# Performance work log

Hardware: AMD Instinct MI355X
Metric: run time of the kernel (lower is better)

Reference implementation:

```python
import jax, jax.numpy as jnp
import numpy as np

B, P, K_NN, HEADS = 4, 2048, 30, 3
N = B * P


def knn_nbr(feat):
    """Per-cloud exact KNN (no self), returns [N, K_NN+1] global neighbor idx, self appended last.
    Matches torch_geometric knn_graph (loop=False) followed by GATConv add_self_loops=True."""
    f = feat.reshape(B, P, -1)
    sq = jnp.sum(f * f, axis=-1)  # [B,P]
    d = sq[:, :, None] + sq[:, None, :] - 2.0 * jnp.einsum('bpc,bqc->bpq', f, f)
    d = d + jnp.eye(P, dtype=f.dtype)[None] * 1e9  # exclude self
    idx = jax.lax.top_k(-d, K_NN)[1]  # [B,P,K_NN] nearest neighbors
    idx = (idx + (jnp.arange(B) * P)[:, None, None]).reshape(N, K_NN)
    return jnp.concatenate([idx, jnp.arange(N)[:, None]], axis=1)  # self-loop last


def gat(xf, nbr, W, a_src, a_dst, bias):
    """PyG GATConv (v1, concat=True, negative_slope=0.2). nbr: [N,K] incoming sources per node."""
    H, F = a_src.shape
    xh = (xf @ W).reshape(N, H, F)
    s = jnp.sum(xh * a_src, axis=-1)  # [N,H] source scores
    t = jnp.sum(xh * a_dst, axis=-1)  # [N,H] target scores
    e = jax.nn.leaky_relu(s[nbr] + t[:, None, :], 0.2)  # [N,K,H]
    alpha = jax.nn.softmax(e, axis=1)  # edge-softmax over incoming edges
    out = jnp.einsum('nkh,nkhf->nhf', alpha, xh[nbr])
    return out.reshape(N, H * F) + bias


def setup_inputs() -> dict:
    key = jax.random.key(0)
    ks = jax.random.split(key, 48)
    w = lambda k, shape: (jax.random.normal(k, shape, jnp.float32) * 0.1)
    H = HEADS
    inp = {
        'x': jax.random.normal(ks[0], (N, 3), jnp.float32),
        'pos': jax.random.normal(ks[1], (N, 3), jnp.float32),
        'batch': (jnp.arange(N) // P).astype(jnp.int32),
        'w1': w(ks[2], (6, 64 * H)), 'as1': w(ks[3], (H, 64)), 'ad1': w(ks[4], (H, 64)), 'b1': w(ks[5], (64 * H,)),
        'ml1w': w(ks[6], (64 * H, 64)), 'ml1b': w(ks[7], (64,)),
        'w2': w(ks[8], (70, 64 * H)), 'as2': w(ks[9], (H, 64)), 'ad2': w(ks[10], (H, 64)), 'b2': w(ks[11], (64 * H,)),
        'ml2w': w(ks[12], (64 * H, 64)), 'ml2b': w(ks[13], (64,)),
        'w3': w(ks[14], (134, 64 * H)), 'as3': w(ks[15], (H, 64)), 'ad3': w(ks[16], (H, 64)), 'b3': w(ks[17], (64 * H,)),
        'ml3w': w(ks[18], (64 * H, 64)), 'ml3b': w(ks[19], (64,)),
        'w4': w(ks[20], (198, 128 * H)), 'as4': w(ks[21], (H, 128)), 'ad4': w(ks[22], (H, 128)), 'b4': w(ks[23], (128 * H,)),
        'ml4w': w(ks[24], (128 * H, 128)), 'ml4b': w(ks[25], (128,)),
        # fe_mlp: 326 -> 1024 -> 1024 (plain last)
        'few1': w(ks[26], (326, 1024)), 'feb1': w(ks[27], (1024,)),
        'few2': w(ks[28], (1024, 1024)), 'feb2': w(ks[29], (1024,)),
        # head mlp: 1350 -> 256 -> 256 -> 128 -> 50
        'mw1': w(ks[30], (1350, 256)), 'mb1': w(ks[31], (256,)),
        'mw2': w(ks[32], (256, 256)), 'mb2': w(ks[33], (256,)),
        'mw3': w(ks[34], (256, 128)), 'mb3': w(ks[35], (128,)),
        'mw4': w(ks[36], (128, 50)), 'mb4': w(ks[37], (50,)),
    }
    return inp


def reference(x, pos, batch,
              w1, as1, ad1, b1, ml1w, ml1b,
              w2, as2, ad2, b2, ml2w, ml2b,
              w3, as3, ad3, b3, ml3w, ml3b,
              w4, as4, ad4, b4, ml4w, ml4b,
              few1, feb1, few2, feb2,
              mw1, mb1, mw2, mb2, mw3, mb3, mw4, mb4):
    x0 = jnp.concatenate([x, pos], axis=-1)  # [N,6]
    nbr = knn_nbr(x0)
    x1 = gat(x0, nbr, w1, as1, ad1, b1) @ ml1w + ml1b  # [N,64]
    nbr = knn_nbr(x1)
    x2 = gat(jnp.concatenate([x0, x1], 1), nbr, w2, as2, ad2, b2) @ ml2w + ml2b
    nbr = knn_nbr(x2)
    x3 = gat(jnp.concatenate([x0, x1, x2], 1), nbr, w3, as3, ad3, b3) @ ml3w + ml3b
    nbr = knn_nbr(x2)  # faithful to source: 4th graph also built from x2
    x4 = gat(jnp.concatenate([x0, x1, x2, x3], 1), nbr, w4, as4, ad4, b4) @ ml4w + ml4b
    link4 = jnp.concatenate([x0, x1, x2, x3, x4], axis=-1)  # [N,326]
    h = jax.nn.relu(link4 @ few1 + feb1) @ few2 + feb2  # [N,1024]
    g = jnp.max(h, axis=0, keepdims=True)  # global feature (dropout=eval identity)
    lg = jnp.concatenate([link4, jnp.broadcast_to(g, (N, h.shape[1]))], axis=1)
    h = jax.nn.relu(lg @ mw1 + mb1)
    h = jax.nn.relu(h @ mw2 + mb2)
    h = jax.nn.relu(h @ mw3 + mb3)
    out = h @ mw4 + mb4
    return jax.nn.log_softmax(out, axis=1)
```

## Files before the change

kernel.cpp:

```cpp
#include <hip/hip_runtime.h>
#include <hip/hip_bf16.h>
#include <hip/amd_detail/amd_hip_vector_types.h>

#define NPTS 8192
#define PP 2048
#define KNN 30
#define KTOT 31
#define HEADS 3
#define LDH 352
#define NSEG 9
#define LDZ 200
#define LDZB3 200
#define LDZB4 392

typedef __attribute__((ext_vector_type(8))) short short8;
typedef __attribute__((ext_vector_type(4))) float floatx4;
typedef __attribute__((ext_vector_type(4))) unsigned int uint4_t;
typedef unsigned short ushort_t;
typedef unsigned int uint_t;

__device__ inline ushort_t f2bs(float v) {
    __hip_bfloat16 b = __float2bfloat16(v);
    return *reinterpret_cast<ushort_t*>(&b);
}
__device__ inline float bs2f(ushort_t u) {
    __hip_bfloat16 b = *reinterpret_cast<__hip_bfloat16*>(&u);
    return __bfloat162float(b);
}
__device__ inline void split2(float v, ushort_t& h, ushort_t& l) {
    h = f2bs(v);
    l = f2bs(v - bs2f(h));
}
__device__ inline uint_t fenc(float f) {
    uint_t b = __float_as_uint(f);
    return (b & 0x80000000u) ? ~b : (b | 0x80000000u);
}
__device__ inline float fdec(uint_t e) {
    return __uint_as_float((e & 0x80000000u) ? (e & 0x7FFFFFFFu) : ~e);
}

__global__ void k_build_x0(const float* __restrict__ x, const float* __restrict__ pos,
                           ushort_t* __restrict__ lh, ushort_t* __restrict__ ll) {
    int i = blockIdx.x * blockDim.x + threadIdx.x;
    if (i >= NPTS * 6) return;
    int n = i / 6, c = i % 6;
    float v = (c < 3) ? x[n * 3 + c] : pos[n * 3 + (c - 3)];
    ushort_t h, l; split2(v, h, l);
    lh[(size_t)n * LDH + c] = h;
    ll[(size_t)n * LDH + c] = l;
}

template<int F_>
__device__ inline void combine_body(const float* __restrict__ w, const float* __restrict__ mlw,
                                    const float* __restrict__ as_, const float* __restrict__ ad,
                                    const float* __restrict__ b, const float* __restrict__ mlb,
                                    float* __restrict__ wc, float* __restrict__ bc,
                                    int K_, int lb) {
    constexpr int NC = 3 * F_ + 6;
    constexpr int JG = 128 / F_;
    constexpr int RG = 8 / JG;
    int h = lb % 3, kb = lb / 3;
    int k0 = kb * 8, KS = min(8, K_ - k0);
    int tid = threadIdx.x;
    int j = tid % F_, rg = tid / F_;
    __shared__ float ws[8][F_];
    __shared__ float ms[32][F_];
    __shared__ float bav[3][F_];
    for (int idx = tid; idx < 8 * F_; idx += 128) {
        int r = idx / F_, f = idx % F_;
        ws[r][f] = (r < KS) ? w[(size_t)(k0 + r) * (3 * F_) + h * F_ + f] : 0.f;
    }
    for (int f = tid; f < F_; f += 128) {
        bav[0][f] = b[h * F_ + f];
        bav[1][f] = as_[h * F_ + f];
        bav[2][f] = ad[h * F_ + f];
    }
    __syncthreads();
    const float* mh = mlw + (size_t)h * F_ * F_;
    float acc[RG] = {};
    float bacc = 0.f;
    for (int f0 = 0; f0 < F_; f0 += 32) {
        for (int idx = tid; idx < 32 * F_; idx += 128) {
            int u = idx / F_, jj = idx % F_;
            ms[u][jj] = mh[(size_t)(f0 + u) * F_ + jj];
        }
        __syncthreads();
#pragma unroll
        for (int u = 0; u < 32; u++) {
            float m = ms[u][j];
#pragma unroll
            for (int r = 0; r < RG; r++)
                acc[r] += ws[rg * RG + r][f0 + u] * m;
            if (rg == 0) bacc += bav[0][f0 + u] * m;
        }
        __syncthreads();
    }
#pragma unroll
    for (int r = 0; r < RG; r++) {
        int k = k0 + rg * RG + r;
        if (k < K_) wc[(size_t)k * NC + h * F_ + j] = acc[r];
    }
    if (kb == 0 && rg == 0)
        atomicAdd(&bc[j], bacc + (h == 0 ? mlb[j] : 0.f));
    if (tid < 16) {
        int r = tid >> 1, sc = tid & 1;
        if (r < KS) {
            float s = 0.f;
#pragma unroll
            for (int f = 0; f < F_; f++) s += ws[r][f] * bav[1 + sc][f];
            wc[(size_t)(k0 + r) * NC + 3 * F_ + sc * 3 + h] = s;
        }
    }
}

struct CAll {
    const float *w[4], *mlw[4], *as_[4], *ad[4], *b[4], *mlb[4];
    float *wc[4], *bc[4];
    int K[4], t0[4], t64;
};
__global__ __launch_bounds__(128)
void k_combine_all(CAll a) {
    int bt = blockIdx.x;
    if (bt < a.t64) {
        int si = 0;
#pragma unroll
        for (int i = 1; i < 3; i++) if (bt >= a.t0[i]) si = i;
        combine_body<64>(a.w[si], a.mlw[si], a.as_[si], a.ad[si], a.b[si], a.mlb[si],
                         a.wc[si], a.bc[si], a.K[si], bt - a.t0[si]);
    } else {
        combine_body<128>(a.w[3], a.mlw[3], a.as_[3], a.ad[3], a.b[3], a.mlb[3],
                          a.wc[3], a.bc[3], a.K[3], bt - a.t64);
    }
}

__global__ void k_tw1(const float* __restrict__ x, const float* __restrict__ pos,
                      const float* __restrict__ wc, float* __restrict__ z) {
    int t = blockIdx.x * blockDim.x + threadIdx.x;
    if (t >= NPTS * 198) return;
    int n = t / 198, j = t % 198;
    float acc = 0.f;
#pragma unroll
    for (int c = 0; c < 3; c++) {
        acc += x[n * 3 + c] * wc[c * 198 + j];
        acc += pos[n * 3 + c] * wc[(3 + c) * 198 + j];
    }
    z[(size_t)n * LDZ + j] = acc;
}

struct WArgs {
    const float* src[NSEG];
    ushort_t* dst[NSEG];
    int K[NSEG], N[NSEG], Kp[NSEG], t0[NSEG];
};
__global__ void k_wsplit_all(WArgs a) {
    int bt = blockIdx.x;
    int si = 0;
#pragma unroll
    for (int i = 1; i < NSEG; i++) if (bt >= a.t0[i]) si = i;
    int t = bt - a.t0[si];
    int K_ = a.K[si], N_ = a.N[si], Kp = a.Kp[si];
    const float* src = a.src[si];
    ushort_t* dh = a.dst[si];
    ushort_t* dl = dh + (size_t)Kp * N_;
    int tX = (N_ + 31) >> 5;
    int k0 = (t / tX) * 32, n0 = (t % tX) * 32;
    __shared__ float tt[32][33];
    int c = threadIdx.x & 31, r8 = threadIdx.x >> 5;
#pragma unroll
    for (int i = 0; i < 4; i++) {
        int r = r8 + i * 8;
        int k = k0 + r, n = n0 + c;
        tt[r][c] = (k < K_ && n < N_) ? src[(size_t)k * N_ + n] : 0.f;
    }
    __syncthreads();
#pragma unroll
    for (int i = 0; i < 4; i++) {
        int r = r8 + i * 8;
        int n = n0 + r, k = k0 + c;
        if (n < N_) {
            float v = tt[c][r];
            ushort_t h, l; split2(v, h, l);
            dh[(size_t)n * Kp + k] = h;
            dl[(size_t)n * Kp + k] = l;
        }
    }
}

template<int MT, int NT>
__global__ __launch_bounds__(256)
void k_mgemm1(const ushort_t* __restrict__ A, int lda,
              const ushort_t* __restrict__ W, int ldw,
              float* __restrict__ Cf, int ldc,
              ushort_t* __restrict__ Ch, int ldh,
              int Ndim, int K,
              const float* __restrict__ bias1, const float* __restrict__ bias2,
              int relu, int lsm, uint_t* __restrict__ gmax) {
    constexpr int MTW = MT / 64;
    constexpr int NTT = NT / 16;
    __shared__ ushort_t As[2][MT * 40];
    __shared__ ushort_t Bs[2][NT * 40];
    __shared__ uint_t smax[NT];
    int tid = threadIdx.x;
    int w = tid >> 6, lane = tid & 63;
    int quad = lane >> 4, l16 = lane & 15;
    int m0 = blockIdx.x * MT, n0 = blockIdx.y * NT;
    uint4_t pa[MT / 64], pb[NT / 64];
    auto prefetch = [&](int k0) {
#pragma unroll
        for (int rep = 0; rep < MT / 64; rep++) {
            int idx = tid + rep * 256;
            int row = idx >> 2, q = idx & 3;
            pa[rep] = *(const uint4_t*)(A + (size_t)(m0 + row) * lda + k0 + q * 8);
        }
#pragma unroll
        for (int rep = 0; rep < NT / 64; rep++) {
            int idx = tid + rep * 256;
            int row = idx >> 2, q = idx & 3;
            uint4_t v = {0, 0, 0, 0};
            if (n0 + row < Ndim) v = *(const uint4_t*)(W + (size_t)(n0 + row) * ldw + k0 + q * 8);
            pb[rep] = v;
        }
    };
    auto stage = [&](int buf) {
#pragma unroll
        for (int rep = 0; rep < MT / 64; rep++) {
            int idx = tid + rep * 256;
            int row = idx >> 2, q = idx & 3;
            *(uint4_t*)&As[buf][row * 40 + q * 8] = pa[rep];
        }
#pragma unroll
        for (int rep = 0; rep < NT / 64; rep++) {
            int idx = tid + rep * 256;
            int row = idx >> 2, q = idx & 3;
            *(uint4_t*)&Bs[buf][row * 40 + q * 8] = pb[rep];
        }
    };
    if (gmax) {
        for (int idx = tid; idx < NT; idx += 256) smax[idx] = 0u;
    }
    floatx4 acc[MTW][NTT] = {};
    prefetch(0);
    stage(0);
    __syncthreads();
    int cur = 0;
    for (int k0 = 0; k0 < K; k0 += 32) {
        bool more = (k0 + 32 < K);
        if (more) prefetch(k0 + 32);
        short8 ah[MTW];
#pragma unroll
        for (int mt = 0; mt < MTW; mt++) {
            int r = w * (MT / 4) + mt * 16 + l16;
            ah[mt] = *(short8*)&As[cur][r * 40 + quad * 8];
        }
#pragma unroll
        for (int nt = 0; nt < NTT; nt++) {
            int r = nt * 16 + l16;
            short8 bh = *(short8*)&Bs[cur][r * 40 + quad * 8];
#pragma unroll
            for (int mt = 0; mt < MTW; mt++)
                acc[mt][nt] = __builtin_amdgcn_mfma_f32_16x16x32_bf16(ah[mt], bh, acc[mt][nt], 0, 0, 0);
        }
        if (more) stage(cur ^ 1);
        __syncthreads();
        cur ^= 1;
    }
    if (lsm) {
#pragma unroll
        for (int mt = 0; mt < MTW; mt++) {
#pragma unroll
            for (int r = 0; r < 4; r++) {
                float vv[NTT];
                float mrow = -3e38f;
#pragma unroll
                for (int nt = 0; nt < NTT; nt++) {
                    int n = n0 + nt * 16 + l16;
                    float val = (n < Ndim) ? acc[mt][nt][r] + bias1[n] : -3e38f;
                    vv[nt] = val;
                    mrow = fmaxf(mrow, val);
                }
#pragma unroll
                for (int off = 8; off >= 1; off >>= 1)
                    mrow = fmaxf(mrow, __shfl_xor(mrow, off, 64));
                float s = 0.f;
#pragma unroll
                for (int nt = 0; nt < NTT; nt++)
                    if (vv[nt] > -1e38f) s += expf(vv[nt] - mrow);
#pragma unroll
                for (int off = 8; off >= 1; off >>= 1)
                    s += __shfl_xor(s, off, 64);
                float lse = mrow + logf(s);
                int m = m0 + w * (MT / 4) + mt * 16 + quad * 4 + r;
#pragma unroll
                for (int nt = 0; nt < NTT; nt++) {
                    int n = n0 + nt * 16 + l16;
                    if (n < Ndim) Cf[(size_t)m * ldc + n] = vv[nt] - lse;
                }
            }
        }
        return;
    }
    if (gmax) {
#pragma unroll
        for (int mt = 0; mt < MTW; mt++) {
#pragma unroll
            for (int nt = 0; nt < NTT; nt++) {
#pragma unroll
                for (int r = 0; r < 4; r++) {
                    float v = acc[mt][nt][r] + bias1[nt * 16 + l16 + n0];
                    atomicMax(&smax[nt * 16 + l16], fenc(v));
                }
            }
        }
        __syncthreads();
        for (int idx = tid; idx < NT; idx += 256)
            atomicMax(&gmax[n0 + idx], smax[idx]);
        return;
    }
#pragma unroll
    for (int mt = 0; mt < MTW; mt++) {
#pragma unroll
        for (int nt = 0; nt < NTT; nt++) {
#pragma unroll
            for (int r = 0; r < 4; r++) {
                int m = m0 + w * (MT / 4) + mt * 16 + quad * 4 + r;
                int n = n0 + nt * 16 + l16;
                if (n < Ndim) {
                    float v = acc[mt][nt][r];
                    if (bias1) v += bias1[n];
                    if (bias2) v += bias2[n];
                    if (relu && v < 0.f) v = 0.f;
                    if (Cf) Cf[(size_t)m * ldc + n] = v;
                    if (Ch) Ch[(size_t)m * ldh + n] = f2bs(v);
                }
            }
        }
    }
}

__global__ __launch_bounds__(256)
void k_head34(const ushort_t* __restrict__ A, int lda,
              const ushort_t* __restrict__ W3, int ldw3,
              const ushort_t* __restrict__ W4, int ldw4,
              const float* __restrict__ mb3, const float* __restrict__ mb4,
              float* __restrict__ out) {
    __shared__ ushort_t As[64 * 40];
    __shared__ ushort_t Bs[128 * 40];
    __shared__ ushort_t C1[64 * 136];
    int tid = threadIdx.x;
    int w = tid >> 6, lane = tid & 63;
    int quad = lane >> 4, l16 = lane & 15;
    int m0 = blockIdx.x * 64;
    floatx4 acc[8] = {};
    for (int k0 = 0; k0 < 256; k0 += 32) {
        {
            int row = tid >> 2, q = tid & 3;
            *(uint4_t*)&As[row * 40 + q * 8] =
                *(const uint4_t*)(A + (size_t)(m0 + row) * lda + k0 + q * 8);
#pragma unroll
            for (int rep = 0; rep < 2; rep++) {
                int idx = tid + rep * 256;
                int br = idx >> 2, bq = idx & 3;
                *(uint4_t*)&Bs[br * 40 + bq * 8] =
                    *(const uint4_t*)(W3 + (size_t)br * ldw3 + k0 + bq * 8);
            }
        }
        __syncthreads();
        short8 ah = *(short8*)&As[(w * 16 + l16) * 40 + quad * 8];
#pragma unroll
        for (int nt = 0; nt < 8; nt++) {
            short8 bh = *(short8*)&Bs[(nt * 16 + l16) * 40 + quad * 8];
            acc[nt] = __builtin_amdgcn_mfma_f32_16x16x32_bf16(ah, bh, acc[nt], 0, 0, 0);
        }
        __syncthreads();
    }
#pragma unroll
    for (int nt = 0; nt < 8; nt++) {
#pragma unroll
        for (int r = 0; r < 4; r++) {
            int rowl = w * 16 + quad * 4 + r;
            int col = nt * 16 + l16;
            float v = acc[nt][r] + mb3[col];
            if (v < 0.f) v = 0.f;
            C1[rowl * 136 + col] = f2bs(v);
        }
    }
    __syncthreads();
    floatx4 acc2[4] = {};
    for (int k0 = 0; k0 < 128; k0 += 32) {
        {
            int row = tid >> 2, q = tid & 3;
            uint4_t v = {0, 0, 0, 0};
            if (row < 50) v = *(const uint4_t*)(W4 + (size_t)row * ldw4 + k0 + q * 8);
            *(uint4_t*)&Bs[row * 40 + q * 8] = v;
        }
        __syncthreads();
        short8 ah = *(short8*)&C1[(w * 16 + l16) * 136 + k0 + quad * 8];
#pragma unroll
        for (int nt = 0; nt < 4; nt++) {
            short8 bh = *(short8*)&Bs[(nt * 16 + l16) * 40 + quad * 8];
            acc2[nt] = __builtin_amdgcn_mfma_f32_16x16x32_bf16(ah, bh, acc2[nt], 0, 0, 0);
        }
        __syncthreads();
    }
#pragma unroll
    for (int r = 0; r < 4; r++) {
        float vv[4];
        float mrow = -3e38f;
#pragma unroll
        for (int nt = 0; nt < 4; nt++) {
            int n = nt * 16 + l16;
            float val = (n < 50) ? acc2[nt][r] + mb4[n] : -3e38f;
            vv[nt] = val;
            mrow = fmaxf(mrow, val);
        }
#pragma unroll
        for (int off = 8; off >= 1; off >>= 1)
            mrow = fmaxf(mrow, __shfl_xor(mrow, off, 64));
        float s = 0.f;
#pragma unroll
        for (int nt = 0; nt < 4; nt++)
            if (vv[nt] > -1e38f) s += expf(vv[nt] - mrow);
#pragma unroll
        for (int off = 8; off >= 1; off >>= 1)
            s += __shfl_xor(s, off, 64);
        float lse = mrow + logf(s);
        int m = m0 + w * 16 + quad * 4 + r;
#pragma unroll
        for (int nt = 0; nt < 4; nt++) {
            int n = nt * 16 + l16;
            if (n < 50) out[(size_t)m * 50 + n] = vv[nt] - lse;
        }
    }
}

__global__ __launch_bounds__(256)
void k_mgemm3(const ushort_t* __restrict__ Ah, const ushort_t* __restrict__ Al, int lda,
              const ushort_t* __restrict__ Wh, const ushort_t* __restrict__ Wl, int ldw,
              float* __restrict__ Cf, int ldc,
              int Ndim, int K) {
    constexpr int NTT = 4;
    __shared__ ushort_t AsH[64 * 40], BsH[64 * 40], AsL[64 * 40], BsL[64 * 40];
    int tid = threadIdx.x;
    int w = tid >> 6, lane = tid & 63;
    int quad = lane >> 4, l16 = lane & 15;
    int m0 = blockIdx.y * 64, n0 = blockIdx.x * 64;
    floatx4 acc[NTT] = {};
    for (int k0 = 0; k0 < K; k0 += 32) {
        {
            int row = tid >> 2, q = tid & 3;
            size_t go = (size_t)(m0 + row) * lda + k0 + q * 8;
            *(uint4_t*)&AsH[row * 40 + q * 8] = *(const uint4_t*)(Ah + go);
            *(uint4_t*)&AsL[row * 40 + q * 8] = *(const uint4_t*)(Al + go);
            uint4_t vh = {0, 0, 0, 0}, vl = {0, 0, 0, 0};
            size_t gw = (size_t)(n0 + row) * ldw + k0 + q * 8;
            if (n0 + row < Ndim) { vh = *(const uint4_t*)(Wh + gw); vl = *(const uint4_t*)(Wl + gw); }
            *(uint4_t*)&BsH[row * 40 + q * 8] = vh;
            *(uint4_t*)&BsL[row * 40 + q * 8] = vl;
        }
        __syncthreads();
        short8 ah, al;
        {
            int r = w * 16 + l16;
            ah = *(short8*)&AsH[r * 40 + quad * 8];
            al = *(short8*)&AsL[r * 40 + quad * 8];
        }
#pragma unroll
        for (int nt = 0; nt < NTT; nt++) {
            int r = nt * 16 + l16;
            short8 bh = *(short8*)&BsH[r * 40 + quad * 8];
            short8 bl = *(short8*)&BsL[r * 40 + quad * 8];
            acc[nt] = __builtin_amdgcn_mfma_f32_16x16x32_bf16(ah, bh, acc[nt], 0, 0, 0);
            acc[nt] = __builtin_amdgcn_mfma_f32_16x16x32_bf16(ah, bl, acc[nt], 0, 0, 0);
            acc[nt] = __builtin_amdgcn_mfma_f32_16x16x32_bf16(al, bh, acc[nt], 0, 0, 0);
        }
        __syncthreads();
    }
#pragma unroll
    for (int nt = 0; nt < NTT; nt++) {
#pragma unroll
        for (int r = 0; r < 4; r++) {
            int m = m0 + w * 16 + quad * 4 + r;
            int n = n0 + nt * 16 + l16;
            if (n < Ndim) Cf[(size_t)m * ldc + n] = acc[nt][r];
        }
    }
}

__global__ __launch_bounds__(256)
void k_mdist(const ushort_t* __restrict__ Lh, const ushort_t* __restrict__ Ll,
             int co, int C, uint_t* __restrict__ keys) {
    __shared__ ushort_t AsH[128 * 40], AsL[128 * 40], BsH[64 * 40], BsL[64 * 40];
    __shared__ float sqa[128], sqb[64];
    int tid = threadIdx.x;
    int w = tid >> 6, lane = tid & 63;
    int quad = lane >> 4, l16 = lane & 15;
    int b = blockIdx.z, cb = b * PP;
    int i0 = blockIdx.y * 128, j0 = blockIdx.x * 64;
    floatx4 acc[2][4] = {};
    float sacc = 0.f;
    for (int k0 = 0; k0 < C; k0 += 32) {
#pragma unroll
        for (int rep = 0; rep < 8; rep++) {
            int d = tid + rep * 256;
            int row = d >> 4, c2 = d & 15;
            size_t gi = ((size_t)(cb + i0 + row) * LDH + co + k0 + c2 * 2) >> 1;
            *(uint_t*)&AsH[row * 40 + c2 * 2] = ((const uint_t*)Lh)[gi];
            *(uint_t*)&AsL[row * 40 + c2 * 2] = ((const uint_t*)Ll)[gi];
        }
#pragma unroll
        for (int rep = 0; rep < 4; rep++) {
            int d = tid + rep * 256;
            int row = d >> 4, c2 = d & 15;
            size_t gi = ((size_t)(cb + j0 + row) * LDH + co + k0 + c2 * 2) >> 1;
            *(uint_t*)&BsH[row * 40 + c2 * 2] = ((const uint_t*)Lh)[gi];
            *(uint_t*)&BsL[row * 40 + c2 * 2] = ((const uint_t*)Ll)[gi];
        }
        __syncthreads();
        if (tid < 128) {
#pragma unroll
            for (int kk = 0; kk < 16; kk++) {
                uint_t ph = *(uint_t*)&AsH[tid * 40 + kk * 2];
                uint_t pl = *(uint_t*)&AsL[tid * 40 + kk * 2];
                float v0 = bs2f((ushort_t)(ph & 0xFFFFu)) + bs2f((ushort_t)(pl & 0xFFFFu));
                sacc += v0 * v0;
                float v1 = bs2f((ushort_t)(ph >> 16)) + bs2f((ushort_t)(pl >> 16));
                sacc += v1 * v1;
            }
        } else if (tid < 192) {
            int row = tid - 128;
#pragma unroll
            for (int kk = 0; kk < 16; kk++) {
                uint_t ph = *(uint_t*)&BsH[row * 40 + kk * 2];
                uint_t pl = *(uint_t*)&BsL[row * 40 + kk * 2];
                float v0 = bs2f((ushort_t)(ph & 0xFFFFu)) + bs2f((ushort_t)(pl & 0xFFFFu));
                sacc += v0 * v0;
                float v1 = bs2f((ushort_t)(ph >> 16)) + bs2f((ushort_t)(pl >> 16));
                sacc += v1 * v1;
            }
        }
        short8 ah[2], al[2];
#pragma unroll
        for (int mt = 0; mt < 2; mt++) {
            int r = w * 32 + mt * 16 + l16;
            ah[mt] = *(short8*)&AsH[r * 40 + quad * 8];
            al[mt] = *(short8*)&AsL[r * 40 + quad * 8];
        }
#pragma unroll
        for (int nt = 0; nt < 4; nt++) {
            int r = nt * 16 + l16;
            short8 bh = *(short8*)&BsH[r * 40 + quad * 8];
            short8 bl = *(short8*)&BsL[r * 40 + quad * 8];
#pragma unroll
            for (int mt = 0; mt < 2; mt++) {
                acc[mt][nt] = __builtin_amdgcn_mfma_f32_16x16x32_bf16(ah[mt], bh, acc[mt][nt], 0, 0, 0);
                acc[mt][nt] = __builtin_amdgcn_mfma_f32_16x16x32_bf16(ah[mt], bl, acc[mt][nt], 0, 0, 0);
                acc[mt][nt] = __builtin_amdgcn_mfma_f32_16x16x32_bf16(al[mt], bh, acc[mt][nt], 0, 0, 0);
            }
        }
        __syncthreads();
    }
    if (tid < 128) sqa[tid] = sacc;
    else if (tid < 192) sqb[tid - 128] = sacc;
    __syncthreads();
#pragma unroll
    for (int mt = 0; mt < 2; mt++) {
#pragma unroll
        for (int nt = 0; nt < 4; nt++) {
#pragma unroll
            for (int r = 0; r < 4; r++) {
                int li = w * 32 + mt * 16 + quad * 4 + r;
                int lj = nt * 16 + l16;
                int il = i0 + li, jl = j0 + lj;
                float dd = sqa[li] + sqb[lj] - 2.f * acc[mt][nt][r];
                dd = (il == jl) ? 3e9f : fmaxf(dd, 0.f);
                uint_t key = (__float_as_uint(dd) & 0xFFFFF800u) | (uint_t)jl;
                keys[(size_t)(cb + il) * PP + jl] = key;
            }
        }
    }
}

__global__ __launch_bounds__(256)
void k_topk(const uint_t* __restrict__ keys, int* __restrict__ nbr) {
    int r = blockIdx.x * 4 + (threadIdx.x >> 6);
    int lane = threadIdx.x & 63;
    int base = (r / PP) * PP;
    const uint_t* row = keys + (size_t)r * PP;
    uint_t v[32];
#pragma unroll
    for (int j = 0; j < 8; j++)
        *(uint4_t*)&v[j * 4] = *(const uint4_t*)(row + lane * 4 + j * 256);
    uint_t g[8];
#pragma unroll
    for (int j = 0; j < 8; j++)
        g[j] = min(min(v[j * 4], v[j * 4 + 1]), min(v[j * 4 + 2], v[j * 4 + 3]));
    uint_t lv = g[0];
#pragma unroll
    for (int j = 1; j < 8; j++) lv = min(lv, g[j]);
    for (int sel = 0; sel < KNN; sel++) {
        uint_t bk = lv;
#pragma unroll
        for (int off = 32; off > 0; off >>= 1)
            bk = min(bk, (uint_t)__shfl_xor((int)bk, off, 64));
        uint_t bks = __builtin_amdgcn_readfirstlane(bk);
        if (lane == 0) nbr[r * KTOT + sel] = base + (int)(bks & 0x7FFu);
        int grp = (int)((bks & 0x7FFu) >> 8);
#pragma unroll
        for (int jj = 0; jj < 8; jj++)
            if (grp == jj) {
#pragma unroll
                for (int t = 0; t < 4; t++)
                    v[jj * 4 + t] = (v[jj * 4 + t] == bks) ? 0xFFFFFFFFu : v[jj * 4 + t];
                g[jj] = min(min(v[jj * 4], v[jj * 4 + 1]), min(v[jj * 4 + 2], v[jj * 4 + 3]));
            }
        lv = g[0];
#pragma unroll
        for (int j = 1; j < 8; j++) lv = min(lv, g[j]);
    }
    if (lane == 0) nbr[r * KTOT + KNN] = r;
}

template<int F, int NN>
__global__ __launch_bounds__(192)
void k_gat2(const float* __restrict__ z, int ldz,
            const int* __restrict__ nbr,
            const float* __restrict__ bc,
            ushort_t* __restrict__ dh, ushort_t* __restrict__ dl) {
    constexpr int TPN = 3 * F / 4;
    __shared__ int srcs[NN][KTOT];
    __shared__ float alpha[NN][96];
    __shared__ float part[NN][2][F];
    int tid = threadIdx.x;
    if (tid < NN * KTOT) {
        int u = tid / KTOT, k = tid % KTOT;
        int t = blockIdx.x * NN + u;
        int node = (t & 3) * PP + (t >> 2);
        srcs[u][k] = nbr[node * KTOT + k];
    }
    __syncthreads();
#pragma unroll
    for (int u2 = 0; u2 < NN; u2 += 2) {
        int u = u2 + tid / 96;
        int r = tid % 96, h = r >> 5, k = r & 31;
        int t = blockIdx.x * NN + u;
        int node = (t & 3) * PP + (t >> 2);
        float e = -3e38f;
        if (k < KTOT) {
            float sv = z[(size_t)srcs[u][k] * ldz + 3 * F + h];
            float tv = z[(size_t)node * ldz + 3 * F + 3 + h];
            e = sv + tv;
            if (e < 0.f) e *= 0.2f;
        }
        float m = e;
#pragma unroll
        for (int off = 16; off >= 1; off >>= 1)
            m = fmaxf(m, __shfl_xor(m, off, 32));
        float ex = (k < KTOT) ? expf(e - m) : 0.f;
        float s = ex;
#pragma unroll
        for (int off = 16; off >= 1; off >>= 1)
            s += __shfl_xor(s, off, 32);
        alpha[u][h * 32 + k] = ex / s;
    }
    __syncthreads();
    {
        int u = tid / TPN, r = tid % TPN;
        int h = r / (F / 4), jq = r % (F / 4);
        const float* zb = z + h * F + jq * 4;
        floatx4 a0 = {0.f, 0.f, 0.f, 0.f}, a1 = {0.f, 0.f, 0.f, 0.f};
#pragma unroll
        for (int k = 0; k < KTOT; k += 2) {
            float a = alpha[u][h * 32 + k];
            floatx4 p = *(const floatx4*)(zb + (size_t)srcs[u][k] * ldz);
            a0 += p * a;
            if (k + 1 < KTOT) {
                float a2 = alpha[u][h * 32 + k + 1];
                floatx4 p2 = *(const floatx4*)(zb + (size_t)srcs[u][k + 1] * ldz);
                a1 += p2 * a2;
            }
        }
        floatx4 av = a0 + a1;
        if (h > 0)
            *(floatx4*)&part[u][h - 1][jq * 4] = av;
        __syncthreads();
        if (h == 0) {
            int t = blockIdx.x * NN + u;
            int node = (t & 3) * PP + (t >> 2);
            int j0 = jq * 4;
            floatx4 p0 = *(const floatx4*)&part[u][0][j0];
            floatx4 p1 = *(const floatx4*)&part[u][1][j0];
            floatx4 bcv = *(const floatx4*)&bc[j0];
            floatx4 v = av + p0 + p1 + bcv;
            ushort_t hh[4], ll[4];
#pragma unroll
            for (int q = 0; q < 4; q++) split2(v[q], hh[q], ll[q]);
            *(uint_t*)&dh[(size_t)node * LDH + j0] = (uint_t)hh[0] | ((uint_t)hh[1] << 16);
            *(uint_t*)&dh[(size_t)node * LDH + j0 + 2] = (uint_t)hh[2] | ((uint_t)hh[3] << 16);
            if (dl) {
                *(uint_t*)&dl[(size_t)node * LDH + j0] = (uint_t)ll[0] | ((uint_t)ll[1] << 16);
                *(uint_t*)&dl[(size_t)node * LDH + j0 + 2] = (uint_t)ll[2] | ((uint_t)ll[3] << 16);
            }
        }
    }
}

template<int F, int NN>
__global__ __launch_bounds__(192)
void k_gat2b(const ushort_t* __restrict__ z, int ldz,
             const int* __restrict__ nbr,
             const float* __restrict__ bc,
             ushort_t* __restrict__ dh) {
    constexpr int TPN = 3 * F / 8;
    __shared__ int srcs[NN][KTOT];
    __shared__ float alpha[NN][96];
    __shared__ float part[NN][2][F];
    int tid = threadIdx.x;
    for (int idx = tid; idx < NN * KTOT; idx += 192) {
        int u = idx / KTOT, k = idx % KTOT;
        int t = blockIdx.x * NN + u;
        int node = (t & 3) * PP + (t >> 2);
        srcs[u][k] = nbr[node * KTOT + k];
    }
    __syncthreads();
#pragma unroll
    for (int u2 = 0; u2 < NN; u2 += 2) {
        int u = u2 + tid / 96;
        int r = tid % 96, h = r >> 5, k = r & 31;
        int t = blockIdx.x * NN + u;
        int node = (t & 3) * PP + (t >> 2);
        float e = -3e38f;
        if (k < KTOT) {
            float sv = bs2f(z[(size_t)srcs[u][k] * ldz + 3 * F + h]);
            float tv = bs2f(z[(size_t)node * ldz + 3 * F + 3 + h]);
            e = sv + tv;
            if (e < 0.f) e *= 0.2f;
        }
        float m = e;
#pragma unroll
        for (int off = 16; off >= 1; off >>= 1)
            m = fmaxf(m, __shfl_xor(m, off, 32));
        float ex = (k < KTOT) ? expf(e - m) : 0.f;
        float s = ex;
#pragma unroll
        for (int off = 16; off >= 1; off >>= 1)
            s += __shfl_xor(s, off, 32);
        alpha[u][h * 32 + k] = ex / s;
    }
    __syncthreads();
    {
        int u = tid / TPN, r = tid % TPN;
        int h = r / (F / 8), jo = r % (F / 8);
        const ushort_t* zb = z + h * F + jo * 8;
        float a[8] = {};
        for (int k = 0; k < KTOT; k++) {
            float al = alpha[u][h * 32 + k];
            short8 v = *(const short8*)(zb + (size_t)srcs[u][k] * ldz);
#pragma unroll
            for (int q = 0; q < 8; q++)
                a[q] += al * bs2f((ushort_t)v[q]);
        }
        if (h > 0) {
#pragma unroll
            for (int q = 0; q < 8; q++) part[u][h - 1][jo * 8 + q] = a[q];
        }
        __syncthreads();
        if (h == 0) {
            int t = blockIdx.x * NN + u;
            int node = (t & 3) * PP + (t >> 2);
            int j0 = jo * 8;
#pragma unroll
            for (int q2 = 0; q2 < 4; q2++) {
                float v0 = a[q2 * 2] + part[u][0][j0 + q2 * 2] + part[u][1][j0 + q2 * 2] + bc[j0 + q2 * 2];
                float v1 = a[q2 * 2 + 1] + part[u][0][j0 + q2 * 2 + 1] + part[u][1][j0 + q2 * 2 + 1] + bc[j0 + q2 * 2 + 1];
                *(uint_t*)&dh[(size_t)node * LDH + j0 + q2 * 2] =
                    (uint_t)f2bs(v0) | ((uint_t)f2bs(v1) << 16);
            }
        }
    }
}

__global__ void k_gproj(const uint_t* __restrict__ genc,
                        const float* __restrict__ mw1,
                        const float* __restrict__ mb1,
                        float* __restrict__ gproj) {
    __shared__ float gs[128];
    int kb = blockIdx.x;
    int t = threadIdx.x;
    if (t < 128) gs[t] = fdec(genc[kb * 128 + t]);
    __syncthreads();
    float acc = (kb == 0) ? mb1[t] : 0.f;
    for (int k = 0; k < 128; k++)
        acc += gs[k] * mw1[(size_t)(326 + kb * 128 + k) * 256 + t];
    atomicAdd(&gproj[t], acc);
}

struct WT { ushort_t *h, *l; int kp; };

extern "C" void kernel_launch(void* const* d_in, const int* in_sizes, int n_in,
                              void* d_out, int out_size, void* d_ws, size_t ws_size,
                              hipStream_t stream) {
    (void)in_sizes; (void)n_in; (void)out_size; (void)ws_size;
    const float* x    = (const float*)d_in[0];
    const float* pos  = (const float*)d_in[1];
    const float* w1   = (const float*)d_in[3];
    const float* as1  = (const float*)d_in[4];
    const float* ad1  = (const float*)d_in[5];
    const float* b1   = (const float*)d_in[6];
    const float* ml1w = (const float*)d_in[7];
    const float* ml1b = (const float*)d_in[8];
    const float* w2   = (const float*)d_in[9];
    const float* as2  = (const float*)d_in[10];
    const float* ad2  = (const float*)d_in[11];
    const float* b2   = (const float*)d_in[12];
    const float* ml2w = (const float*)d_in[13];
    const float* ml2b = (const float*)d_in[14];
    const float* w3   = (const float*)d_in[15];
    const float* as3  = (const float*)d_in[16];
    const float* ad3  = (const float*)d_in[17];
    const float* b3   = (const float*)d_in[18];
    const float* ml3w = (const float*)d_in[19];
    const float* ml3b = (const float*)d_in[20];
    const float* w4   = (const float*)d_in[21];
    const float* as4  = (const float*)d_in[22];
    const float* ad4  = (const float*)d_in[23];
    const float* b4   = (const float*)d_in[24];
    const float* ml4w = (const float*)d_in[25];
    const float* ml4b = (const float*)d_in[26];
    const float* few1 = (const float*)d_in[27];
    const float* feb1 = (const float*)d_in[28];
    const float* few2 = (const float*)d_in[29];
    const float* feb2 = (const float*)d_in[30];
    const float* mw1  = (const float*)d_in[31];
    const float* mb1  = (const float*)d_in[32];
    const float* mw2  = (const float*)d_in[33];
    const float* mb2  = (const float*)d_in[34];
    const float* mw3  = (const float*)d_in[35];
    const float* mb3  = (const float*)d_in[36];
    const float* mw4  = (const float*)d_in[37];
    const float* mb4  = (const float*)d_in[38];

    float* Wb = (float*)d_ws;
    size_t off = 0;
    auto alloc = [&](size_t n) { float* p = Wb + off; off += (n + 63) & ~(size_t)63; return p; };

    float*    dist = alloc((size_t)NPTS * PP);
    ushort_t* l4h  = (ushort_t*)alloc((size_t)NPTS * LDH / 2);
    ushort_t* l4l  = (ushort_t*)alloc((size_t)NPTS * LDH / 2);
    uint_t* genc = (uint_t*)alloc(1024);
    float* gproj = alloc(256);
    float* bcp = alloc(320);
    float* bc1 = bcp, *bc2 = bcp + 64, *bc3 = bcp + 128, *bc4 = bcp + 192;
    int*   nbr   = (int*)alloc((size_t)NPTS * KTOT);
    ushort_t* wtpool = (ushort_t*)alloc(1742336);
    float* wc1 = alloc(6 * 198);
    float* wc2 = alloc(70 * 198);
    float* wc3 = alloc(134 * 198);
    float* wc4 = alloc(198 * 390);

    char* d0 = (char*)dist;
    uint_t*   dkey = (uint_t*)dist;
    float*    z    = dist;
    ushort_t* zb   = (ushort_t*)dist;
    ushort_t* hah  = (ushort_t*)d0;
    ushort_t* bBh  = (ushort_t*)(d0 + (size_t)NPTS * 1024 * 2);
    ushort_t* bAh = (ushort_t*)d0;

    hipMemsetAsync(l4h, 0, ((size_t)NPTS * LDH + 1600) * 4, stream);

    {
        CAll ca;
        const float* ws_[4] = {w1, w2, w3, w4};
        const float* mlws[4] = {ml1w, ml2w, ml3w, ml4w};
        const float* ass[4] = {as1, as2, as3, as4};
        const float* ads[4] = {ad1, ad2, ad3, ad4};
        const float* bs_[4] = {b1, b2, b3, b4};
        const float* mlbs[4] = {ml1b, ml2b, ml3b, ml4b};
        float* wcs[4] = {wc1, wc2, wc3, wc4};
        float* bcs[4] = {bc1, bc2, bc3, bc4};
        int Ks[4] = {6, 70, 134, 198};
        int t = 0;
        for (int i = 0; i < 4; i++) {
            ca.w[i] = ws_[i]; ca.mlw[i] = mlws[i]; ca.as_[i] = ass[i]; ca.ad[i] = ads[i];
            ca.b[i] = bs_[i]; ca.mlb[i] = mlbs[i]; ca.wc[i] = wcs[i]; ca.bc[i] = bcs[i];
            ca.K[i] = Ks[i];
            if (i < 3) { ca.t0[i] = t; t += ((Ks[i] + 7) / 8) * 3; }
        }
        ca.t64 = t;
        int total = t + 25 * 3;
        k_combine_all<<<total, 128, 0, stream>>>(ca);
    }

    WArgs wa;
    WT wt[NSEG];
    {
        const float* srcs[NSEG] = {wc2, wc3, wc4, few1, few2, mw1, mw2, mw3, mw4};
        int Ks[NSEG] = {70, 134, 198, 326, 1024, 326, 256, 256, 128};
        int Ns[NSEG] = {198, 198, 390, 1024, 1024, 256, 256, 128, 50};
        size_t wo = 0; int tiles = 0;
        for (int i = 0; i < NSEG; i++) {
            int kp = (Ks[i] + 31) & ~31;
            wa.src[i] = srcs[i];
            wa.dst[i] = wtpool + wo;
            wa.K[i] = Ks[i]; wa.N[i] = Ns[i]; wa.Kp[i] = kp;
            wa.t0[i] = tiles;
            wt[i] = { wtpool + wo, wtpool + wo + (size_t)kp * Ns[i], kp };
            wo += (size_t)2 * kp * Ns[i];
            tiles += (kp / 32) * ((Ns[i] + 31) / 32);
        }
        k_wsplit_all<<<tiles, 256, 0, stream>>>(wa);
    }
    WT tw2 = wt[0], tw3 = wt[1], tw4 = wt[2], tfe1 = wt[3], tfe2 = wt[4],
       tmw1 = wt[5], tmw2 = wt[6], tmw3 = wt[7], tmw4 = wt[8];

    auto mg3 = [&](const ushort_t* Ah, const ushort_t* Al, int lda, WT t,
                   float* Cf, int ldc, int Nd, int K) {
        dim3 g((Nd + 63) / 64, NPTS / 64);
        k_mgemm3<<<g, 256, 0, stream>>>(Ah, Al, lda, t.h, t.l, t.kp, Cf, ldc, Nd, K);
    };
    auto mg1 = [&](int MT, int NT, const ushort_t* Ah, int lda, WT t,
                   float* Cf, int ldc, ushort_t* Ch, int ldhh,
                   int Nd, int K, const float* bb1, const float* bb2,
                   int relu, int lsm, uint_t* gmax) {
        dim3 g(NPTS / MT, (Nd + NT - 1) / NT);
        if (MT == 128 && NT == 128)
            k_mgemm1<128, 128><<<g, 256, 0, stream>>>(Ah, lda, t.h, t.kp, Cf, ldc, Ch, ldhh, Nd, K,
                bb1, bb2, relu, lsm, gmax);
        else if (MT == 128)
            k_mgemm1<128, 64><<<g, 256, 0, stream>>>(Ah, lda, t.h, t.kp, Cf, ldc, Ch, ldhh, Nd, K,
                bb1, bb2, relu, lsm, gmax);
        else
            k_mgemm1<64, 64><<<g, 256, 0, stream>>>(Ah, lda, t.h, t.kp, Cf, ldc, Ch, ldhh, Nd, K,
                bb1, bb2, relu, lsm, gmax);
    };

    dim3 dgrid(PP / 64, PP / 128, 4);
    k_build_x0<<<(NPTS * 6 + 255) / 256, 256, 0, stream>>>(x, pos, l4h, l4l);

    k_mdist<<<dgrid, 256, 0, stream>>>(l4h, l4l, 0, 6, dkey);
    k_topk<<<NPTS / 4, 256, 0, stream>>>(dkey, nbr);
    k_tw1<<<(NPTS * 198 + 255) / 256, 256, 0, stream>>>(x, pos, wc1, z);
    k_gat2<64, 4><<<NPTS / 4, 192, 0, stream>>>(z, LDZ, nbr, bc1, l4h + 6, l4l + 6);

    k_mdist<<<dgrid, 256, 0, stream>>>(l4h, l4l, 6, 64, dkey);
    k_topk<<<NPTS / 4, 256, 0, stream>>>(dkey, nbr);
    mg3(l4h, l4l, LDH, tw2, z, LDZ, 198, 70);
    k_gat2<64, 4><<<NPTS / 4, 192, 0, stream>>>(z, LDZ, nbr, bc2, l4h + 70, l4l + 70);

    k_mdist<<<dgrid, 256, 0, stream>>>(l4h, l4l, 70, 64, dkey);
    k_topk<<<NPTS / 4, 256, 0, stream>>>(dkey, nbr);
    mg1(128, 64, l4h, LDH, tw3, nullptr, 0, zb, LDZB3, 198, 134, nullptr, nullptr, 0, 0, nullptr);
    k_gat2b<64, 8><<<NPTS / 8, 192, 0, stream>>>(zb, LDZB3, nbr, bc3, l4h + 134);

    mg1(128, 64, l4h, LDH, tw4, nullptr, 0, zb, LDZB4, 390, 198, nullptr, nullptr, 0, 0, nullptr);
    k_gat2b<128, 4><<<NPTS / 4, 192, 0, stream>>>(zb, LDZB4, nbr, bc4, l4h + 198);

    mg1(128, 128, l4h, LDH, tfe1, nullptr, 0, hah, 1024, 1024, 326, feb1, nullptr, 1, 0, nullptr);
    mg1(128, 128, hah, 1024, tfe2, nullptr, 0, nullptr, 0, 1024, 1024, feb2, nullptr, 0, 0, genc);
    k_gproj<<<8, 256, 0, stream>>>(genc, mw1, mb1, gproj);

    mg1(128, 64, l4h, LDH, tmw1, nullptr, 0, bAh, 256, 256, 326, nullptr, gproj, 1, 0, nullptr);
    mg1(128, 64, bAh, 256, tmw2, nullptr, 0, bBh, 256, 256, 256, mb2, nullptr, 1, 0, nullptr);
    k_head34<<<NPTS / 64, 256, 0, stream>>>(bBh, 256, tmw3.h, tmw3.kp, tmw4.h, tmw4.kp,
                                            mb3, mb4, (float*)d_out);
}
```

Measured before the change: 503.9 us.

## Fuse all four MLP head layers into one per-tile kernel

Replaces the two separate GEMM launches for the first two head layers plus the layer-3/4 kernel with a single kernel that keeps each 64-row tile's intermediate activations in shared memory through all four layers and the log-softmax. This removes two launches and the global-memory round trips of the 256-wide bf16 intermediates. The cost is larger shared memory (Bs grows to 256 rows, C to 64x264), 16 accumulators per thread, and only 128 blocks, which can reduce occupancy and parallelism for the larger first two GEMMs.

```diff
diff --git a/kernel.cpp b/kernel.cpp
--- a/kernel.cpp
+++ b/kernel.cpp
@@ -338,97 +338,172 @@
 }
 
 __global__ __launch_bounds__(256)
-void k_head34(const ushort_t* __restrict__ A, int lda,
-              const ushort_t* __restrict__ W3, int ldw3,
-              const ushort_t* __restrict__ W4, int ldw4,
-              const float* __restrict__ mb3, const float* __restrict__ mb4,
-              float* __restrict__ out) {
+void k_head_all(const ushort_t* __restrict__ A, int lda,
+                const ushort_t* __restrict__ W1, int ldw1,
+                const ushort_t* __restrict__ W2, int ldw2,
+                const ushort_t* __restrict__ W3, int ldw3,
+                const ushort_t* __restrict__ W4, int ldw4,
+                const float* __restrict__ gproj, const float* __restrict__ mb2,
+                const float* __restrict__ mb3, const float* __restrict__ mb4,
+                float* __restrict__ out) {
     __shared__ ushort_t As[64 * 40];
-    __shared__ ushort_t Bs[128 * 40];
-    __shared__ ushort_t C1[64 * 136];
+    __shared__ ushort_t Bs[256 * 40];
+    __shared__ ushort_t C[64 * 264];
     int tid = threadIdx.x;
     int w = tid >> 6, lane = tid & 63;
     int quad = lane >> 4, l16 = lane & 15;
     int m0 = blockIdx.x * 64;
-    floatx4 acc[8] = {};
-    for (int k0 = 0; k0 < 256; k0 += 32) {
-        {
-            int row = tid >> 2, q = tid & 3;
-            *(uint4_t*)&As[row * 40 + q * 8] =
-                *(const uint4_t*)(A + (size_t)(m0 + row) * lda + k0 + q * 8);
-#pragma unroll
-            for (int rep = 0; rep < 2; rep++) {
-                int idx = tid + rep * 256;
-                int br = idx >> 2, bq = idx & 3;
-                *(uint4_t*)&Bs[br * 40 + bq * 8] =
-                    *(const uint4_t*)(W3 + (size_t)br * ldw3 + k0 + bq * 8);
-            }
-        }
-        __syncthreads();
-        short8 ah = *(short8*)&As[(w * 16 + l16) * 40 + quad * 8];
+    {
+        floatx4 acc[16] = {};
+        for (int k0 = 0; k0 < 326; k0 += 32) {
+            {
+                int row = tid >> 2, q = tid & 3;
+                *(uint4_t*)&As[row * 40 + q * 8] =
+                    *(const uint4_t*)(A + (size_t)(m0 + row) * lda + k0 + q * 8);
+#pragma unroll
+                for (int rep = 0; rep < 4; rep++) {
+                    int idx = tid + rep * 256;
+                    int br = idx >> 2, bq = idx & 3;
+                    *(uint4_t*)&Bs[br * 40 + bq * 8] =
+                        *(const uint4_t*)(W1 + (size_t)br * ldw1 + k0 + bq * 8);
+                }
+            }
+            __syncthreads();
+            short8 ah = *(short8*)&As[(w * 16 + l16) * 40 + quad * 8];
+#pragma unroll
+            for (int nt = 0; nt < 16; nt++) {
+                short8 bh = *(short8*)&Bs[(nt * 16 + l16) * 40 + quad * 8];
+                acc[nt] = __builtin_amdgcn_mfma_f32_16x16x32_bf16(ah, bh, acc[nt], 0, 0, 0);
+            }
+            __syncthreads();
+        }
+#pragma unroll
+        for (int nt = 0; nt < 16; nt++) {
+#pragma unroll
+            for (int r = 0; r < 4; r++) {
+                int rowl = w * 16 + quad * 4 + r;
+                int col = nt * 16 + l16;
+                float v = acc[nt][r] + gproj[col];
+                if (v < 0.f) v = 0.f;
+                C[rowl * 264 + col] = f2bs(v);
+            }
+        }
+        __syncthreads();
+    }
+    {
+        floatx4 acc[16] = {};
+        for (int k0 = 0; k0 < 256; k0 += 32) {
+            {
+#pragma unroll
+                for (int rep = 0; rep < 4; rep++) {
+                    int idx = tid + rep * 256;
+                    int br = idx >> 2, bq = idx & 3;
+                    *(uint4_t*)&Bs[br * 40 + bq * 8] =
+                        *(const uint4_t*)(W2 + (size_t)br * ldw2 + k0 + bq * 8);
+                }
+            }
+            __syncthreads();
+            short8 ah = *(short8*)&C[(w * 16 + l16) * 264 + k0 + quad * 8];
+#pragma unroll
+            for (int nt = 0; nt < 16; nt++) {
+                short8 bh = *(short8*)&Bs[(nt * 16 + l16) * 40 + quad * 8];
+                acc[nt] = __builtin_amdgcn_mfma_f32_16x16x32_bf16(ah, bh, acc[nt], 0, 0, 0);
+            }
+            __syncthreads();
+        }
+#pragma unroll
+        for (int nt = 0; nt < 16; nt++) {
+#pragma unroll
+            for (int r = 0; r < 4; r++) {
+                int rowl = w * 16 + quad * 4 + r;
+                int col = nt * 16 + l16;
+                float v = acc[nt][r] + mb2[col];
+                if (v < 0.f) v = 0.f;
+                C[rowl * 264 + col] = f2bs(v);
+            }
+        }
+        __syncthreads();
+    }
+    {
+        floatx4 acc[8] = {};
+        for (int k0 = 0; k0 < 256; k0 += 32) {
+            {
+#pragma unroll
+                for (int rep = 0; rep < 2; rep++) {
+                    int idx = tid + rep * 256;
+                    int br = idx >> 2, bq = idx & 3;
+                    *(uint4_t*)&Bs[br * 40 + bq * 8] =
+                        *(const uint4_t*)(W3 + (size_t)br * ldw3 + k0 + bq * 8);
+                }
+            }
+            __syncthreads();
+            short8 ah = *(short8*)&C[(w * 16 + l16) * 264 + k0 + quad * 8];
+#pragma unroll
+            for (int nt = 0; nt < 8; nt++) {
+                short8 bh = *(short8*)&Bs[(nt * 16 + l16) * 40 + quad * 8];
+                acc[nt] = __builtin_amdgcn_mfma_f32_16x16x32_bf16(ah, bh, acc[nt], 0, 0, 0);
+            }
+            __syncthreads();
+        }
 #pragma unroll
         for (int nt = 0; nt < 8; nt++) {
-            short8 bh = *(short8*)&Bs[(nt * 16 + l16) * 40 + quad * 8];
-            acc[nt] = __builtin_amdgcn_mfma_f32_16x16x32_bf16(ah, bh, acc[nt], 0, 0, 0);
-        }
-        __syncthreads();
-    }
-#pragma unroll
-    for (int nt = 0; nt < 8; nt++) {
+#pragma unroll
+            for (int r = 0; r < 4; r++) {
+                int rowl = w * 16 + quad * 4 + r;
+                int col = nt * 16 + l16;
+                float v = acc[nt][r] + mb3[col];
+                if (v < 0.f) v = 0.f;
+                C[rowl * 264 + col] = f2bs(v);
+            }
+        }
+        __syncthreads();
+    }
+    {
+        floatx4 acc[4] = {};
+        for (int k0 = 0; k0 < 128; k0 += 32) {
+            {
+                int row = tid >> 2, q = tid & 3;
+                uint4_t v = {0, 0, 0, 0};
+                if (row < 50) v = *(const uint4_t*)(W4 + (size_t)row * ldw4 + k0 + q * 8);
+                *(uint4_t*)&Bs[row * 40 + q * 8] = v;
+            }
+            __syncthreads();
+            short8 ah = *(short8*)&C[(w * 16 + l16) * 264 + k0 + quad * 8];
+#pragma unroll
+            for (int nt = 0; nt < 4; nt++) {
+                short8 bh = *(short8*)&Bs[(nt * 16 + l16) * 40 + quad * 8];
+                acc[nt] = __builtin_amdgcn_mfma_f32_16x16x32_bf16(ah, bh, acc[nt], 0, 0, 0);
+            }
+            __syncthreads();
+        }
 #pragma unroll
         for (int r = 0; r < 4; r++) {
-            int rowl = w * 16 + quad * 4 + r;
-            int col = nt * 16 + l16;
-            float v = acc[nt][r] + mb3[col];
-            if (v < 0.f) v = 0.f;
-            C1[rowl * 136 + col] = f2bs(v);
-        }
-    }
-    __syncthreads();
-    floatx4 acc2[4] = {};
-    for (int k0 = 0; k0 < 128; k0 += 32) {
-        {
-            int row = tid >> 2, q = tid & 3;
-            uint4_t v = {0, 0, 0, 0};
-            if (row < 50) v = *(const uint4_t*)(W4 + (size_t)row * ldw4 + k0 + q * 8);
-            *(uint4_t*)&Bs[row * 40 + q * 8] = v;
-        }
-        __syncthreads();
-        short8 ah = *(short8*)&C1[(w * 16 + l16) * 136 + k0 + quad * 8];
-#pragma unroll
-        for (int nt = 0; nt < 4; nt++) {
-            short8 bh = *(short8*)&Bs[(nt * 16 + l16) * 40 + quad * 8];
-            acc2[nt] = __builtin_amdgcn_mfma_f32_16x16x32_bf16(ah, bh, acc2[nt], 0, 0, 0);
-        }
-        __syncthreads();
-    }
-#pragma unroll
-    for (int r = 0; r < 4; r++) {
-        float vv[4];
-        float mrow = -3e38f;
-#pragma unroll
-        for (int nt = 0; nt < 4; nt++) {
-            int n = nt * 16 + l16;
-            float val = (n < 50) ? acc2[nt][r] + mb4[n] : -3e38f;
-            vv[nt] = val;
-            mrow = fmaxf(mrow, val);
-        }
-#pragma unroll
-        for (int off = 8; off >= 1; off >>= 1)
-            mrow = fmaxf(mrow, __shfl_xor(mrow, off, 64));
-        float s = 0.f;
-#pragma unroll
-        for (int nt = 0; nt < 4; nt++)
-            if (vv[nt] > -1e38f) s += expf(vv[nt] - mrow);
-#pragma unroll
-        for (int off = 8; off >= 1; off >>= 1)
-            s += __shfl_xor(s, off, 64);
-        float lse = mrow + logf(s);
-        int m = m0 + w * 16 + quad * 4 + r;
-#pragma unroll
-        for (int nt = 0; nt < 4; nt++) {
-            int n = nt * 16 + l16;
-            if (n < 50) out[(size_t)m * 50 + n] = vv[nt] - lse;
+            float vv[4];
+            float mrow = -3e38f;
+#pragma unroll
+            for (int nt = 0; nt < 4; nt++) {
+                int n = nt * 16 + l16;
+                float val = (n < 50) ? acc[nt][r] + mb4[n] : -3e38f;
+                vv[nt] = val;
+                mrow = fmaxf(mrow, val);
+            }
+#pragma unroll
+            for (int off = 8; off >= 1; off >>= 1)
+                mrow = fmaxf(mrow, __shfl_xor(mrow, off, 64));
+            float s = 0.f;
+#pragma unroll
+            for (int nt = 0; nt < 4; nt++)
+                if (vv[nt] > -1e38f) s += expf(vv[nt] - mrow);
+#pragma unroll
+            for (int off = 8; off >= 1; off >>= 1)
+                s += __shfl_xor(s, off, 64);
+            float lse = mrow + logf(s);
+            int m = m0 + w * 16 + quad * 4 + r;
+#pragma unroll
+            for (int nt = 0; nt < 4; nt++) {
+                int n = nt * 16 + l16;
+                if (n < 50) out[(size_t)m * 50 + n] = vv[nt] - lse;
+            }
         }
     }
 }
@@ -862,8 +937,6 @@
     float*    z    = dist;
     ushort_t* zb   = (ushort_t*)dist;
     ushort_t* hah  = (ushort_t*)d0;
-    ushort_t* bBh  = (ushort_t*)(d0 + (size_t)NPTS * 1024 * 2);
-    ushort_t* bAh = (ushort_t*)d0;
 
     hipMemsetAsync(l4h, 0, ((size_t)NPTS * LDH + 1600) * 4, stream);
 
@@ -958,8 +1031,7 @@
     mg1(128, 128, hah, 1024, tfe2, nullptr, 0, nullptr, 0, 1024, 1024, feb2, nullptr, 0, 0, genc);
     k_gproj<<<8, 256, 0, stream>>>(genc, mw1, mb1, gproj);
 
-    mg1(128, 64, l4h, LDH, tmw1, nullptr, 0, bAh, 256, 256, 326, nullptr, gproj, 1, 0, nullptr);
-    mg1(128, 64, bAh, 256, tmw2, nullptr, 0, bBh, 256, 256, 256, mb2, nullptr, 1, 0, nullptr);
-    k_head34<<<NPTS / 64, 256, 0, stream>>>(bBh, 256, tmw3.h, tmw3.kp, tmw4.h, tmw4.kp,
-                                            mb3, mb4, (float*)d_out);
-}
+    k_head_all<<<NPTS / 64, 256, 0, stream>>>(l4h, LDH, tmw1.h, tmw1.kp, tmw2.h, tmw2.kp,
+                                              tmw3.h, tmw3.kp, tmw4.h, tmw4.kp,
+                                              gproj, mb2, mb3, mb4, (float*)d_out);
+}
```

Result: no change. 496.1 us (-1.6%).
